# Kernel tuning notes

Measured on AMD Instinct MI355X. Metric: run time of the kernel, lower is better.

The kernel has to match this reference:

```python
import jax, jax.numpy as jnp
import numpy as np

B, N, T = 64, 196, 32
VOCAB, EMB, HDIM, VDIM, ATT = 32000, 256, 512, 256, 256
SCALE = 0.05


def setup_inputs() -> dict:
    key = jax.random.key(0)
    ks = jax.random.split(key, 12)
    f32 = jnp.float32
    return {
        "V": jax.random.normal(ks[0], (B, N, VDIM), f32),
        "y": jax.random.randint(ks[1], (B, T), 0, VOCAB),
        "embed": jax.random.normal(ks[2], (VOCAB, EMB), f32) * SCALE,
        "W_att": jax.random.normal(ks[3], (HDIM, ATT), f32) * SCALE,
        "U_att": jax.random.normal(ks[4], (VDIM, ATT), f32) * SCALE,
        "v_att": jax.random.normal(ks[5], (ATT,), f32) * SCALE,
        "W_ih": jax.random.normal(ks[6], (EMB + VDIM, 4 * HDIM), f32) * SCALE,
        "W_hh": jax.random.normal(ks[7], (HDIM, 4 * HDIM), f32) * SCALE,
        "b_ih": jnp.zeros((4 * HDIM,), f32),
        "b_hh": jnp.zeros((4 * HDIM,), f32),
        "W_inith": jax.random.normal(ks[8], (VDIM, HDIM), f32) * SCALE,
        "b_inith": jnp.zeros((HDIM,), f32),
        "W_initc": jax.random.normal(ks[9], (VDIM, HDIM), f32) * SCALE,
        "b_initc": jnp.zeros((HDIM,), f32),
        "W_proj": jax.random.normal(ks[10], (HDIM, EMB), f32) * SCALE,
    }


def reference(V, y, embed, W_att, U_att, v_att, W_ih, W_hh, b_ih, b_hh,
              W_inith, b_inith, W_initc, b_initc, W_proj):
    # teacher_forcing=True, sampling_prob=0.0, dropout disabled (eval)
    feat_mean = V.mean(1)                                   # [B, vdim]
    h0 = jnp.tanh(feat_mean @ W_inith + b_inith)            # [B, hdim]
    c0 = jnp.tanh(feat_mean @ W_initc + b_initc)
    Uv = jnp.einsum('bnv,va->bna', V, U_att)                # step-invariant attention keys
    x_seq = embed[y[:, :-1]]                                # [B, T-1, emb] teacher-forced inputs

    def step(carry, x_t):
        h, c = carry
        # additive attention: e = v^T tanh(W h + U V)
        e = jnp.einsum('bna,a->bn', jnp.tanh((h @ W_att)[:, None, :] + Uv), v_att)
        a = jax.nn.softmax(e, axis=1)                       # [B, N]
        ctx = jnp.einsum('bn,bnv->bv', a, V)                # [B, vdim]
        # LSTMCell (torch gate order: i, f, g, o)
        gates = jnp.concatenate([x_t, ctx], -1) @ W_ih + b_ih + h @ W_hh + b_hh
        i, f, g, o = jnp.split(gates, 4, axis=-1)
        c = jax.nn.sigmoid(f) * c + jax.nn.sigmoid(i) * jnp.tanh(g)
        h = jax.nn.sigmoid(o) * jnp.tanh(c)
        logit = (h @ W_proj) @ embed.T                      # [B, vocab]
        return (h, c), logit

    _, logits = jax.lax.scan(step, (h0, c0), jnp.swapaxes(x_seq, 0, 1))
    return jnp.swapaxes(logits, 0, 1)                       # [B, T-1, vocab]
```

## Files before the change

kernel.cpp:

```cpp
#include <hip/hip_runtime.h>
#include <hip/hip_bf16.h>
#include <cstdint>
#include <cstddef>

#define B 64
#define N 196
#define T 32
#define TM1 31
#define VOCAB 32000
#define EMB 256
#define HDIM 512
#define VDIM 256
#define ATT 256
#define G4 2048

__device__ __forceinline__ float fast_tanh(float x){
  x = fminf(fmaxf(x, -15.f), 15.f);
  float e = __expf(2.f*x);
  return (e - 1.f) / (e + 1.f);
}
__device__ __forceinline__ float fast_sig(float x){
  x = fminf(fmaxf(x, -30.f), 30.f);
  return 1.f / (1.f + __expf(-x));
}

__global__ void k_init(const float* __restrict__ V, const float* __restrict__ Wh,
                       const float* __restrict__ bh, const float* __restrict__ Wc,
                       const float* __restrict__ bc, float* __restrict__ h0,
                       float* __restrict__ c0){
  int b = blockIdx.x, tid = threadIdx.x;
  __shared__ float fm[VDIM];
  const float* vb = V + (size_t)b*N*VDIM;
  float s = 0.f;
  for (int n=0;n<N;n++) s += vb[n*VDIM + tid];
  fm[tid] = s * (1.f/196.f);
  __syncthreads();
  for (int j=tid; j<HDIM; j+=256){
    float sh = bh[j], sc = bc[j];
    #pragma unroll 4
    for (int k=0;k<VDIM;k++){
      float f = fm[k];
      sh = fmaf(f, Wh[k*HDIM + j], sh);
      sc = fmaf(f, Wc[k*HDIM + j], sc);
    }
    h0[b*HDIM + j] = fast_tanh(sh);
    c0[b*HDIM + j] = fast_tanh(sc);
  }
}

__global__ void k_uv(const float* __restrict__ V, const float* __restrict__ U,
                     float* __restrict__ Uv){
  int tid = threadIdx.x;
  size_t r0 = (size_t)blockIdx.x * 8;
  __shared__ float vs[8][VDIM];
  for (int i=tid; i<8*VDIM; i+=256)
    vs[i>>8][i&255] = V[r0*VDIM + i];
  __syncthreads();
  float acc[8] = {0,0,0,0,0,0,0,0};
  int a = tid;
  #pragma unroll 4
  for (int k=0;k<VDIM;k++){
    float u = U[k*ATT + a];
    #pragma unroll
    for (int r=0;r<8;r++) acc[r] = fmaf(vs[r][k], u, acc[r]);
  }
  for (int r=0;r<8;r++) Uv[(r0 + r)*ATT + a] = acc[r];
}

__global__ __launch_bounds__(256)
void k_xw(const float* __restrict__ embed, const int* __restrict__ y,
          const float* __restrict__ Wih, const float* __restrict__ bih,
          const float* __restrict__ bhh, float* __restrict__ XWb){
  __shared__ int ys[128];
  __shared__ float Xl[32][129];
  __shared__ float Wl[32][129];
  int tid = threadIdx.x;
  int c0 = blockIdx.x * 128, r0 = blockIdx.y * 128;
  if (tid < 128){
    int r = r0 + tid;
    ys[tid] = (r < TM1*B) ? y[(r & 63)*T + (r >> 6)] : 0;
  }
  int kk = tid & 31, rb = tid >> 5;
  int wk = tid >> 7, wc = tid & 127;
  int tx = tid & 15, ty = tid >> 4;
  float acc[8][8];
  #pragma unroll
  for (int i=0;i<8;i++)
    #pragma unroll
    for (int j=0;j<8;j++) acc[i][j]=0.f;
  for (int kc=0; kc<EMB; kc+=32){
    __syncthreads();
    #pragma unroll
    for (int i=0;i<16;i++){
      Xl[kk][rb + i*8] = embed[(size_t)ys[rb + i*8]*EMB + kc + kk];
      Wl[wk + i*2][wc] = Wih[(size_t)(kc + wk + i*2)*G4 + c0 + wc];
    }
    __syncthreads();
    for (int k=0;k<32;k++){
      float pr_[8], ec[8];
      #pragma unroll
      for (int i=0;i<8;i++) pr_[i] = Xl[k][ty + 16*i];
      #pragma unroll
      for (int j=0;j<8;j++) ec[j] = Wl[k][tx + 16*j];
      #pragma unroll
      for (int i=0;i<8;i++)
        #pragma unroll
        for (int j=0;j<8;j++) acc[i][j] = fmaf(pr_[i], ec[j], acc[i][j]);
    }
  }
  float bb[8];
  #pragma unroll
  for (int j=0;j<8;j++){
    int c = c0 + tx + 16*j;
    bb[j] = bih[c] + bhh[c];
  }
  #pragma unroll
  for (int i=0;i<8;i++){
    int row = r0 + ty + 16*i;
    if (row < TM1*B){
      float* orow = XWb + (size_t)row*G4 + c0;
      #pragma unroll
      for (int j=0;j<8;j++) orow[tx + 16*j] = acc[i][j] + bb[j];
    }
  }
}

__global__ __launch_bounds__(512)
void k_att(const float* __restrict__ V, const float* __restrict__ Uv,
           const float* __restrict__ Wa, const float* __restrict__ va,
           const float* __restrict__ gprev,
           const float* __restrict__ h0, float* __restrict__ c_st,
           float* __restrict__ hwr,
           float* __restrict__ ctx){
  int b = blockIdx.x, tid = threadIdx.x;
  __shared__ float hs[HDIM];
  __shared__ float qs[ATT];
  __shared__ float vat[ATT];
  __shared__ float es[200];
  __shared__ float qp[512];
  __shared__ float redm[8], reds[8];
  __shared__ float sM, sInv;

  if (tid < 256) vat[tid] = va[tid];
  if (gprev){
    const float* grow = gprev + (size_t)b*G4;
    float gi = grow[tid], gf = grow[512+tid], gg = grow[1024+tid], go = grow[1536+tid];
    float c = c_st[b*HDIM + tid];
    c = fmaf(fast_sig(gf), c, fast_sig(gi)*fast_tanh(gg));
    float h = fast_sig(go) * fast_tanh(c);
    c_st[b*HDIM + tid] = c;
    hs[tid] = h;
    hwr[b*HDIM + tid] = h;
  } else {
    hs[tid] = h0[b*HDIM + tid];
  }
  __syncthreads();

  {
    int col = tid & 255, half = tid >> 8;
    int k0 = half*256;
    float s = 0.f;
    #pragma unroll 4
    for (int k=0;k<256;k++) s = fmaf(hs[k0+k], Wa[(size_t)(k0+k)*ATT + col], s);
    qp[tid] = s;
  }
  __syncthreads();
  if (tid < 256) qs[tid] = qp[tid] + qp[tid+256];
  __syncthreads();

  int wv = tid >> 6, lane = tid & 63;
  for (int n=wv; n<N; n+=8){
    const float* uv = Uv + ((size_t)b*N + n)*ATT;
    float s = 0.f;
    #pragma unroll
    for (int a0=0; a0<ATT; a0+=64){
      int a = a0 + lane;
      s = fmaf(vat[a], fast_tanh(qs[a] + uv[a]), s);
    }
    #pragma unroll
    for (int off=32; off>0; off>>=1) s += __shfl_down(s, off, 64);
    if (lane==0) es[n] = s;
  }
  __syncthreads();

  float v = (tid < N) ? es[tid] : -3.0e38f;
  float m = v;
  #pragma unroll
  for (int off=32; off>0; off>>=1) m = fmaxf(m, __shfl_down(m, off, 64));
  if (lane==0) redm[wv] = m;
  __syncthreads();
  if (tid==0){
    float mm = redm[0];
    #pragma unroll
    for (int i=1;i<8;i++) mm = fmaxf(mm, redm[i]);
    sM = mm;
  }
  __syncthreads();
  float p = (tid < N) ? __expf(v - sM) : 0.f;
  float s2 = p;
  #pragma unroll
  for (int off=32; off>0; off>>=1) s2 += __shfl_down(s2, off, 64);
  if (lane==0) reds[wv] = s2;
  __syncthreads();
  if (tid==0){
    float ss = 0.f;
    #pragma unroll
    for (int i=0;i<8;i++) ss += reds[i];
    sInv = 1.f/ss;
  }
  __syncthreads();
  if (tid < N) es[tid] = p * sInv;
  __syncthreads();

  {
    int col = tid & 255, half = tid >> 8;
    int n0 = half*98;
    const float* vb = V + (size_t)b*N*VDIM;
    float s = 0.f;
    #pragma unroll 2
    for (int n=n0; n<n0+98; n++) s = fmaf(es[n], vb[(size_t)n*VDIM + col], s);
    qp[tid] = s;
  }
  __syncthreads();
  if (tid < 256) ctx[b*VDIM + tid] = qp[tid] + qp[tid+256];
}

__global__ __launch_bounds__(256)
void k_gates(const float* __restrict__ ctx, const float* __restrict__ hprev,
             const float* __restrict__ Wih, const float* __restrict__ Whh,
             float* __restrict__ gout){
  int tid = threadIdx.x;
  int ct = blockIdx.x & 31, kcid = blockIdx.x >> 5;
  int c0 = ct * 64;
  __shared__ float zs[64][128];
  for (int i=tid; i<8192; i+=256){
    int b = i >> 7, kk = i & 127;
    float val;
    if (kcid < 2) val = ctx[b*VDIM + kcid*128 + kk];
    else          val = hprev[b*HDIM + kcid*128 - 256 + kk];
    zs[b][kk] = val;
  }
  const float* wbase = (kcid < 2) ? (Wih + (size_t)(256 + kcid*128)*G4)
                                  : (Whh + (size_t)(kcid*128 - 256)*G4);
  __syncthreads();
  int cg = tid & 15, bg = tid >> 4;
  float acc[4][4];
  #pragma unroll
  for (int i=0;i<4;i++)
    #pragma unroll
    for (int j=0;j<4;j++) acc[i][j]=0.f;
  #pragma unroll 4
  for (int k=0;k<128;k++){
    float4 w = *(const float4*)(wbase + (size_t)k*G4 + c0 + cg*4);
    #pragma unroll
    for (int bi=0;bi<4;bi++){
      float zv = zs[bg*4+bi][k];
      acc[bi][0] = fmaf(zv, w.x, acc[bi][0]);
      acc[bi][1] = fmaf(zv, w.y, acc[bi][1]);
      acc[bi][2] = fmaf(zv, w.z, acc[bi][2]);
      acc[bi][3] = fmaf(zv, w.w, acc[bi][3]);
    }
  }
  #pragma unroll
  for (int bi=0;bi<4;bi++){
    int b = bg*4 + bi;
    float* gp = gout + (size_t)b*G4 + c0 + cg*4;
    #pragma unroll
    for (int ci=0;ci<4;ci++) atomicAdd(gp + ci, acc[bi][ci]);
  }
}

__global__ __launch_bounds__(512)
void k_tail(const float* __restrict__ gprev, const float* __restrict__ c_st,
            float* __restrict__ hwr){
  int b = blockIdx.x, tid = threadIdx.x;
  const float* grow = gprev + (size_t)b*G4;
  float gi = grow[tid], gf = grow[512+tid], gg = grow[1024+tid], go = grow[1536+tid];
  float c = c_st[b*HDIM + tid];
  c = fmaf(fast_sig(gf), c, fast_sig(gi)*fast_tanh(gg));
  hwr[b*HDIM + tid] = fast_sig(go) * fast_tanh(c);
}

__global__ void k_proj(const float* __restrict__ H, const float* __restrict__ Wp,
                       float* __restrict__ P){
  int tid = threadIdx.x;
  size_t r0 = (size_t)blockIdx.x * 8;
  __shared__ float hs[8][HDIM];
  for (int i=tid; i<8*HDIM; i+=256)
    hs[i>>9][i&511] = H[r0*HDIM + i];
  __syncthreads();
  float acc[8] = {0,0,0,0,0,0,0,0};
  int e = tid;
  #pragma unroll 4
  for (int k=0;k<HDIM;k++){
    float w = Wp[k*EMB + e];
    #pragma unroll
    for (int r=0;r<8;r++) acc[r] = fmaf(hs[r][k], w, acc[r]);
  }
  for (int r=0;r<8;r++) P[(r0 + r)*EMB + e] = acc[r];
}

__global__ __launch_bounds__(256)
void k_logits(const float* __restrict__ P, const float* __restrict__ E,
              float* __restrict__ out){
  __shared__ float Pl[32][129];
  __shared__ float El[32][129];
  int tid = threadIdx.x;
  int tx = tid & 15, ty = tid >> 4;
  int c0 = blockIdx.x * 128, r0 = blockIdx.y * 128;
  float acc[8][8];
  #pragma unroll
  for (int i=0;i<8;i++)
    #pragma unroll
    for (int j=0;j<8;j++) acc[i][j]=0.f;
  int kk = tid & 31, rb = tid >> 5;
  for (int kc=0; kc<EMB; kc+=32){
    __syncthreads();
    #pragma unroll
    for (int i=0;i<16;i++){
      int pr = r0 + rb + i*8; if (pr > TM1*B-1) pr = TM1*B-1;
      Pl[kk][rb + i*8] = P[(size_t)pr*EMB + kc + kk];
      int er = c0 + rb + i*8;
      El[kk][rb + i*8] = E[(size_t)er*EMB + kc + kk];
    }
    __syncthreads();
    for (int k=0;k<32;k++){
      float pr_[8], ec[8];
      #pragma unroll
      for (int i=0;i<8;i++) pr_[i] = Pl[k][ty + 16*i];
      #pragma unroll
      for (int j=0;j<8;j++) ec[j] = El[k][tx + 16*j];
      #pragma unroll
      for (int i=0;i<8;i++)
        #pragma unroll
        for (int j=0;j<8;j++) acc[i][j] = fmaf(pr_[i], ec[j], acc[i][j]);
    }
  }
  #pragma unroll
  for (int i=0;i<8;i++){
    int row = r0 + ty + 16*i;
    if (row < TM1*B){
      int t = row >> 6, b = row & 63;
      float* orow = out + ((size_t)(b*TM1 + t))*VOCAB + c0;
      #pragma unroll
      for (int j=0;j<8;j++) orow[tx + 16*j] = acc[i][j];
    }
  }
}

extern "C" void kernel_launch(void* const* d_in, const int* in_sizes, int n_in,
                              void* d_out, int out_size, void* d_ws, size_t ws_size,
                              hipStream_t stream){
  const float* V      = (const float*)d_in[0];
  const int*   y      = (const int*)  d_in[1];
  const float* embed  = (const float*)d_in[2];
  const float* W_att  = (const float*)d_in[3];
  const float* U_att  = (const float*)d_in[4];
  const float* v_att  = (const float*)d_in[5];
  const float* W_ih   = (const float*)d_in[6];
  const float* W_hh   = (const float*)d_in[7];
  const float* b_ih   = (const float*)d_in[8];
  const float* b_hh   = (const float*)d_in[9];
  const float* W_inith= (const float*)d_in[10];
  const float* b_inith= (const float*)d_in[11];
  const float* W_initc= (const float*)d_in[12];
  const float* b_initc= (const float*)d_in[13];
  const float* W_proj = (const float*)d_in[14];
  float* out = (float*)d_out;

  float* ws   = (float*)d_ws;
  float* Uv   = ws;
  float* h0   = Uv   + (size_t)B*N*ATT;
  float* c_st = h0   + B*HDIM;
  float* ctx  = c_st + B*HDIM;
  float* Hall = ctx  + B*VDIM;
  float* XWb  = Hall + (size_t)TM1*B*HDIM;
  float* P    = XWb  + (size_t)TM1*B*G4;

  k_init<<<B, 256, 0, stream>>>(V, W_inith, b_inith, W_initc, b_initc, h0, c_st);
  k_uv<<<(B*N)/8, 256, 0, stream>>>(V, U_att, Uv);
  k_xw<<<dim3(16,16), 256, 0, stream>>>(embed, y, W_ih, b_ih, b_hh, XWb);

  for (int t=0;t<TM1;t++){
    const float* gprev = (t==0) ? nullptr : (XWb + (size_t)(t-1)*B*G4);
    float* hwr = (t==0) ? nullptr : (Hall + (size_t)(t-1)*B*HDIM);
    const float* hprev = (t==0) ? h0 : (Hall + (size_t)(t-1)*B*HDIM);
    k_att<<<B, 512, 0, stream>>>(V, Uv, W_att, v_att, gprev, h0, c_st, hwr, ctx);
    k_gates<<<192, 256, 0, stream>>>(ctx, hprev, W_ih, W_hh, XWb + (size_t)t*B*G4);
  }
  k_tail<<<B, 512, 0, stream>>>(XWb + (size_t)30*B*G4, c_st, Hall + (size_t)30*B*HDIM);
  k_proj<<<(TM1*B)/8, 256, 0, stream>>>(Hall, W_proj, P);
  dim3 g(VOCAB/128, (TM1*B + 127)/128);
  k_logits<<<g, 256, 0, stream>>>(P, embed, out);
}
```

Baseline: 3.285 ms.

## Fuse recurrent attention and gate kernels into one persistent cooperative kernel

New measurement: 4.344 ms. 32.2% more time.

```diff
diff --git a/kernel.cpp b/kernel.cpp
--- a/kernel.cpp
+++ b/kernel.cpp
@@ -1,5 +1,5 @@
 #include <hip/hip_runtime.h>
-#include <hip/hip_bf16.h>
+#include <hip/hip_cooperative_groups.h>
 #include <cstdint>
 #include <cstddef>
 
@@ -126,13 +126,15 @@
 }
 
 __global__ __launch_bounds__(512)
-void k_att(const float* __restrict__ V, const float* __restrict__ Uv,
-           const float* __restrict__ Wa, const float* __restrict__ va,
-           const float* __restrict__ gprev,
-           const float* __restrict__ h0, float* __restrict__ c_st,
-           float* __restrict__ hwr,
-           float* __restrict__ ctx){
-  int b = blockIdx.x, tid = threadIdx.x;
+void k_loop(const float* __restrict__ V, const float* __restrict__ Uv,
+            const float* __restrict__ Wa, const float* __restrict__ va,
+            const float* __restrict__ h0, float* __restrict__ c_st,
+            float* __restrict__ ctx, float* __restrict__ Hall,
+            float* __restrict__ XWb, const float* __restrict__ Wih,
+            const float* __restrict__ Whh){
+  cooperative_groups::grid_group grid = cooperative_groups::this_grid();
+  int bid = blockIdx.x, tid = threadIdx.x;
+
   __shared__ float hs[HDIM];
   __shared__ float qs[ATT];
   __shared__ float vat[ATT];
@@ -140,145 +142,150 @@
   __shared__ float qp[512];
   __shared__ float redm[8], reds[8];
   __shared__ float sM, sInv;
-
-  if (tid < 256) vat[tid] = va[tid];
-  if (gprev){
-    const float* grow = gprev + (size_t)b*G4;
+  __shared__ float zs[64][128];
+
+  if (bid < B && tid < 256) vat[tid] = va[tid];
+
+  for (int t=0; t<TM1; t++){
+    if (bid < B){
+      int b = bid;
+      const float* gprev = t ? (XWb + (size_t)(t-1)*B*G4) : nullptr;
+      if (gprev){
+        const float* grow = gprev + (size_t)b*G4;
+        float gi = grow[tid], gf = grow[512+tid], gg = grow[1024+tid], go = grow[1536+tid];
+        float c = c_st[b*HDIM + tid];
+        c = fmaf(fast_sig(gf), c, fast_sig(gi)*fast_tanh(gg));
+        float h = fast_sig(go) * fast_tanh(c);
+        c_st[b*HDIM + tid] = c;
+        hs[tid] = h;
+        Hall[(size_t)(t-1)*B*HDIM + b*HDIM + tid] = h;
+      } else {
+        hs[tid] = h0[b*HDIM + tid];
+      }
+      __syncthreads();
+
+      {
+        int col = tid & 255, half = tid >> 8;
+        int k0 = half*256;
+        float s = 0.f;
+        #pragma unroll 4
+        for (int k=0;k<256;k++) s = fmaf(hs[k0+k], Wa[(size_t)(k0+k)*ATT + col], s);
+        qp[tid] = s;
+      }
+      __syncthreads();
+      if (tid < 256) qs[tid] = qp[tid] + qp[tid+256];
+      __syncthreads();
+
+      int wv = tid >> 6, lane = tid & 63;
+      for (int n=wv; n<N; n+=8){
+        const float* uv = Uv + ((size_t)b*N + n)*ATT;
+        float s = 0.f;
+        #pragma unroll
+        for (int a0=0; a0<ATT; a0+=64){
+          int a = a0 + lane;
+          s = fmaf(vat[a], fast_tanh(qs[a] + uv[a]), s);
+        }
+        #pragma unroll
+        for (int off=32; off>0; off>>=1) s += __shfl_down(s, off, 64);
+        if (lane==0) es[n] = s;
+      }
+      __syncthreads();
+
+      float v = (tid < N) ? es[tid] : -3.0e38f;
+      float m = v;
+      #pragma unroll
+      for (int off=32; off>0; off>>=1) m = fmaxf(m, __shfl_down(m, off, 64));
+      if (lane==0) redm[wv] = m;
+      __syncthreads();
+      if (tid==0){
+        float mm = redm[0];
+        #pragma unroll
+        for (int i=1;i<8;i++) mm = fmaxf(mm, redm[i]);
+        sM = mm;
+      }
+      __syncthreads();
+      float p = (tid < N) ? __expf(v - sM) : 0.f;
+      float s2 = p;
+      #pragma unroll
+      for (int off=32; off>0; off>>=1) s2 += __shfl_down(s2, off, 64);
+      if (lane==0) reds[wv] = s2;
+      __syncthreads();
+      if (tid==0){
+        float ss = 0.f;
+        #pragma unroll
+        for (int i=0;i<8;i++) ss += reds[i];
+        sInv = 1.f/ss;
+      }
+      __syncthreads();
+      if (tid < N) es[tid] = p * sInv;
+      __syncthreads();
+
+      {
+        int col = tid & 255, half = tid >> 8;
+        int n0 = half*98;
+        const float* vb = V + (size_t)b*N*VDIM;
+        float s = 0.f;
+        #pragma unroll 2
+        for (int n=n0; n<n0+98; n++) s = fmaf(es[n], vb[(size_t)n*VDIM + col], s);
+        qp[tid] = s;
+      }
+      __syncthreads();
+      if (tid < 256) ctx[b*VDIM + tid] = qp[tid] + qp[tid+256];
+    }
+    grid.sync();
+
+    if (bid < 192){
+      int ct = bid & 31, kcid = bid >> 5;
+      int c0 = ct * 64;
+      const float* hprev = t ? (Hall + (size_t)(t-1)*B*HDIM) : h0;
+      float* gout = XWb + (size_t)t*B*G4;
+      for (int i=tid; i<8192; i+=512){
+        int bb = i >> 7, kk = i & 127;
+        float val;
+        if (kcid < 2) val = ctx[bb*VDIM + kcid*128 + kk];
+        else          val = hprev[bb*HDIM + kcid*128 - 256 + kk];
+        zs[bb][kk] = val;
+      }
+      const float* wbase = (kcid < 2) ? (Wih + (size_t)(256 + kcid*128)*G4)
+                                      : (Whh + (size_t)(kcid*128 - 256)*G4);
+      __syncthreads();
+      int cg = tid & 15, bg = tid >> 4;
+      float acc[2][4];
+      #pragma unroll
+      for (int i=0;i<2;i++)
+        #pragma unroll
+        for (int j=0;j<4;j++) acc[i][j]=0.f;
+      #pragma unroll 4
+      for (int k=0;k<128;k++){
+        float4 w = *(const float4*)(wbase + (size_t)k*G4 + c0 + cg*4);
+        #pragma unroll
+        for (int bi=0;bi<2;bi++){
+          float zv = zs[bg*2+bi][k];
+          acc[bi][0] = fmaf(zv, w.x, acc[bi][0]);
+          acc[bi][1] = fmaf(zv, w.y, acc[bi][1]);
+          acc[bi][2] = fmaf(zv, w.z, acc[bi][2]);
+          acc[bi][3] = fmaf(zv, w.w, acc[bi][3]);
+        }
+      }
+      #pragma unroll
+      for (int bi=0;bi<2;bi++){
+        int bb = bg*2 + bi;
+        float* gp = gout + (size_t)bb*G4 + c0 + cg*4;
+        #pragma unroll
+        for (int ci=0;ci<4;ci++) atomicAdd(gp + ci, acc[bi][ci]);
+      }
+    }
+    grid.sync();
+  }
+
+  if (bid < B){
+    int b = bid;
+    const float* grow = XWb + (size_t)30*B*G4 + (size_t)b*G4;
     float gi = grow[tid], gf = grow[512+tid], gg = grow[1024+tid], go = grow[1536+tid];
     float c = c_st[b*HDIM + tid];
     c = fmaf(fast_sig(gf), c, fast_sig(gi)*fast_tanh(gg));
-    float h = fast_sig(go) * fast_tanh(c);
-    c_st[b*HDIM + tid] = c;
-    hs[tid] = h;
-    hwr[b*HDIM + tid] = h;
-  } else {
-    hs[tid] = h0[b*HDIM + tid];
-  }
-  __syncthreads();
-
-  {
-    int col = tid & 255, half = tid >> 8;
-    int k0 = half*256;
-    float s = 0.f;
-    #pragma unroll 4
-    for (int k=0;k<256;k++) s = fmaf(hs[k0+k], Wa[(size_t)(k0+k)*ATT + col], s);
-    qp[tid] = s;
-  }
-  __syncthreads();
-  if (tid < 256) qs[tid] = qp[tid] + qp[tid+256];
-  __syncthreads();
-
-  int wv = tid >> 6, lane = tid & 63;
-  for (int n=wv; n<N; n+=8){
-    const float* uv = Uv + ((size_t)b*N + n)*ATT;
-    float s = 0.f;
-    #pragma unroll
-    for (int a0=0; a0<ATT; a0+=64){
-      int a = a0 + lane;
-      s = fmaf(vat[a], fast_tanh(qs[a] + uv[a]), s);
-    }
-    #pragma unroll
-    for (int off=32; off>0; off>>=1) s += __shfl_down(s, off, 64);
-    if (lane==0) es[n] = s;
-  }
-  __syncthreads();
-
-  float v = (tid < N) ? es[tid] : -3.0e38f;
-  float m = v;
-  #pragma unroll
-  for (int off=32; off>0; off>>=1) m = fmaxf(m, __shfl_down(m, off, 64));
-  if (lane==0) redm[wv] = m;
-  __syncthreads();
-  if (tid==0){
-    float mm = redm[0];
-    #pragma unroll
-    for (int i=1;i<8;i++) mm = fmaxf(mm, redm[i]);
-    sM = mm;
-  }
-  __syncthreads();
-  float p = (tid < N) ? __expf(v - sM) : 0.f;
-  float s2 = p;
-  #pragma unroll
-  for (int off=32; off>0; off>>=1) s2 += __shfl_down(s2, off, 64);
-  if (lane==0) reds[wv] = s2;
-  __syncthreads();
-  if (tid==0){
-    float ss = 0.f;
-    #pragma unroll
-    for (int i=0;i<8;i++) ss += reds[i];
-    sInv = 1.f/ss;
-  }
-  __syncthreads();
-  if (tid < N) es[tid] = p * sInv;
-  __syncthreads();
-
-  {
-    int col = tid & 255, half = tid >> 8;
-    int n0 = half*98;
-    const float* vb = V + (size_t)b*N*VDIM;
-    float s = 0.f;
-    #pragma unroll 2
-    for (int n=n0; n<n0+98; n++) s = fmaf(es[n], vb[(size_t)n*VDIM + col], s);
-    qp[tid] = s;
-  }
-  __syncthreads();
-  if (tid < 256) ctx[b*VDIM + tid] = qp[tid] + qp[tid+256];
-}
-
-__global__ __launch_bounds__(256)
-void k_gates(const float* __restrict__ ctx, const float* __restrict__ hprev,
-             const float* __restrict__ Wih, const float* __restrict__ Whh,
-             float* __restrict__ gout){
-  int tid = threadIdx.x;
-  int ct = blockIdx.x & 31, kcid = blockIdx.x >> 5;
-  int c0 = ct * 64;
-  __shared__ float zs[64][128];
-  for (int i=tid; i<8192; i+=256){
-    int b = i >> 7, kk = i & 127;
-    float val;
-    if (kcid < 2) val = ctx[b*VDIM + kcid*128 + kk];
-    else          val = hprev[b*HDIM + kcid*128 - 256 + kk];
-    zs[b][kk] = val;
-  }
-  const float* wbase = (kcid < 2) ? (Wih + (size_t)(256 + kcid*128)*G4)
-                                  : (Whh + (size_t)(kcid*128 - 256)*G4);
-  __syncthreads();
-  int cg = tid & 15, bg = tid >> 4;
-  float acc[4][4];
-  #pragma unroll
-  for (int i=0;i<4;i++)
-    #pragma unroll
-    for (int j=0;j<4;j++) acc[i][j]=0.f;
-  #pragma unroll 4
-  for (int k=0;k<128;k++){
-    float4 w = *(const float4*)(wbase + (size_t)k*G4 + c0 + cg*4);
-    #pragma unroll
-    for (int bi=0;bi<4;bi++){
-      float zv = zs[bg*4+bi][k];
-      acc[bi][0] = fmaf(zv, w.x, acc[bi][0]);
-      acc[bi][1] = fmaf(zv, w.y, acc[bi][1]);
-      acc[bi][2] = fmaf(zv, w.z, acc[bi][2]);
-      acc[bi][3] = fmaf(zv, w.w, acc[bi][3]);
-    }
-  }
-  #pragma unroll
-  for (int bi=0;bi<4;bi++){
-    int b = bg*4 + bi;
-    float* gp = gout + (size_t)b*G4 + c0 + cg*4;
-    #pragma unroll
-    for (int ci=0;ci<4;ci++) atomicAdd(gp + ci, acc[bi][ci]);
-  }
-}
-
-__global__ __launch_bounds__(512)
-void k_tail(const float* __restrict__ gprev, const float* __restrict__ c_st,
-            float* __restrict__ hwr){
-  int b = blockIdx.x, tid = threadIdx.x;
-  const float* grow = gprev + (size_t)b*G4;
-  float gi = grow[tid], gf = grow[512+tid], gg = grow[1024+tid], go = grow[1536+tid];
-  float c = c_st[b*HDIM + tid];
-  c = fmaf(fast_sig(gf), c, fast_sig(gi)*fast_tanh(gg));
-  hwr[b*HDIM + tid] = fast_sig(go) * fast_tanh(c);
+    Hall[(size_t)30*B*HDIM + b*HDIM + tid] = fast_sig(go) * fast_tanh(c);
+  }
 }
 
 __global__ void k_proj(const float* __restrict__ H, const float* __restrict__ Wp,
@@ -381,14 +388,13 @@
   k_uv<<<(B*N)/8, 256, 0, stream>>>(V, U_att, Uv);
   k_xw<<<dim3(16,16), 256, 0, stream>>>(embed, y, W_ih, b_ih, b_hh, XWb);
 
-  for (int t=0;t<TM1;t++){
-    const float* gprev = (t==0) ? nullptr : (XWb + (size_t)(t-1)*B*G4);
-    float* hwr = (t==0) ? nullptr : (Hall + (size_t)(t-1)*B*HDIM);
-    const float* hprev = (t==0) ? h0 : (Hall + (size_t)(t-1)*B*HDIM);
-    k_att<<<B, 512, 0, stream>>>(V, Uv, W_att, v_att, gprev, h0, c_st, hwr, ctx);
-    k_gates<<<192, 256, 0, stream>>>(ctx, hprev, W_ih, W_hh, XWb + (size_t)t*B*G4);
-  }
-  k_tail<<<B, 512, 0, stream>>>(XWb + (size_t)30*B*G4, c_st, Hall + (size_t)30*B*HDIM);
+  void* kargs[] = {
+    (void*)&V, (void*)&Uv, (void*)&W_att, (void*)&v_att, (void*)&h0,
+    (void*)&c_st, (void*)&ctx, (void*)&Hall, (void*)&XWb,
+    (void*)&W_ih, (void*)&W_hh
+  };
+  hipLaunchCooperativeKernel((void*)k_loop, dim3(192), dim3(512), kargs, 0, stream);
+
   k_proj<<<(TM1*B)/8, 256, 0, stream>>>(Hall, W_proj, P);
   dim3 g(VOCAB/128, (TM1*B + 127)/128);
   k_logits<<<g, 256, 0, stream>>>(P, embed, out);
```
